# Optimization experiments

Hardware: AMD Instinct MI355X
Metric: run time of the kernel (lower is better)

## Reference

```python
import jax, jax.numpy as jnp
import numpy as np

B, D, H, L = 2, 1024, 16, 4
BLK = 16                 # block_size == max_text_tokens
MT, MF = 16, 2032        # max_text_tokens, max_font_tokens
S = MT + MF              # 2048
NB = S // BLK            # 128 blocks
V = 490                  # font_vocab_size
HD = D // H              # 64
WIN = 30                 # 3*max_glyph_tokens/block_size = 3*160/16
NGLOB, NRAND = 1, 2      # BigBird global / random blocks
SOS = 0.42


def _make_layout():
    # Deterministic BigBird block layout per head: [H, NB, NB] bool
    rng = np.random.default_rng(0)
    layout = np.zeros((H, NB, NB), dtype=bool)
    layout[:, :NGLOB, :] = True          # global rows
    layout[:, :, :NGLOB] = True          # global cols
    for i in range(NB):                  # sliding window
        layout[:, i, max(0, i - WIN // 2):min(NB, i + WIN // 2 + 1)] = True
    for h in range(H):                   # random blocks
        for i in range(NB):
            layout[h, i, rng.choice(NB, size=NRAND, replace=False)] = True
    return jnp.asarray(layout)


def setup_inputs() -> dict:
    key = jax.random.key(0)
    ks = jax.random.split(key, 16)
    p = lambda k, shape: (0.02 * jax.random.normal(k, shape)).astype(jnp.float32)
    return {
        "text_embeddings": jax.random.normal(ks[0], (B, MT, D), jnp.float32),
        "font_embeddings": jax.random.normal(ks[1], (B, MF, D), jnp.float32),
        "layout": _make_layout(),
        "Wq": p(ks[2], (L, D, D)), "bq": jnp.zeros((L, D), jnp.float32),
        "Wk": p(ks[3], (L, D, D)), "bk": jnp.zeros((L, D), jnp.float32),
        "Wv": p(ks[4], (L, D, D)), "bv": jnp.zeros((L, D), jnp.float32),
        "Wo": p(ks[5], (L, D, D)), "bo": jnp.zeros((L, D), jnp.float32),
        "ln1_g": jnp.ones((L, D), jnp.float32), "ln1_b": jnp.zeros((L, D), jnp.float32),
        "ln2_g": jnp.ones((L, D), jnp.float32), "ln2_b": jnp.zeros((L, D), jnp.float32),
        "W1": p(ks[6], (L, D, 4 * D)), "b1": jnp.zeros((L, 4 * D), jnp.float32),
        "W2": p(ks[7], (L, 4 * D, D)), "b2": jnp.zeros((L, D), jnp.float32),
        "lnf_g": jnp.ones((D,), jnp.float32), "lnf_b": jnp.zeros((D,), jnp.float32),
        "Wout": p(ks[8], (D, V)),
    }


def _ln(x, g, b, eps=1e-5):
    mu = x.mean(-1, keepdims=True)
    var = ((x - mu) ** 2).mean(-1, keepdims=True)
    return (x - mu) * jax.lax.rsqrt(var + eps) * g + b


def _forward(text_embeddings, font_embeddings, layout, Wq, bq, Wk, bk, Wv, bv, Wo, bo,
             ln1_g, ln1_b, ln2_g, ln2_b, W1, b1, W2, b2, lnf_g, lnf_b, Wout):
    sos = jnp.full((B, 1, D), SOS, text_embeddings.dtype)
    x = jnp.concatenate([sos, text_embeddings, font_embeddings[:, :-1, :]], axis=1)  # [B,S,D]
    # token-level mask = block-sparse BigBird layout AND causal -> [H,S,S]
    tok_mask = jnp.repeat(jnp.repeat(layout, BLK, axis=1), BLK, axis=2)
    tok_mask = tok_mask & jnp.tril(jnp.ones((S, S), bool))[None]
    neg = jnp.asarray(-1e9, x.dtype)
    scale = jnp.asarray(1.0 / np.sqrt(HD), x.dtype)

    def layer(x, p):
        wq, bq_, wk, bk_, wv, bv_, wo, bo_, g1, gb1, g2, gb2, w1, bb1, w2, bb2 = p
        q = (x @ wq + bq_).reshape(B, S, H, HD).transpose(0, 2, 1, 3)
        k = (x @ wk + bk_).reshape(B, S, H, HD).transpose(0, 2, 1, 3)
        v = (x @ wv + bv_).reshape(B, S, H, HD).transpose(0, 2, 1, 3)
        scores = jnp.einsum('bhqd,bhkd->bhqk', q, k) * scale
        scores = jnp.where(tok_mask[None], scores, neg)
        probs = jax.nn.softmax(scores, axis=-1)
        a = jnp.einsum('bhqk,bhkd->bhqd', probs, v).transpose(0, 2, 1, 3).reshape(B, S, D)
        a = a @ wo + bo_
        x = _ln(x + a, g1, gb1)                                   # post-norm residual
        m = jax.nn.gelu(x @ w1 + bb1, approximate=False) @ w2 + bb2  # dropout=eval no-op
        x = _ln(x + m, g2, gb2)
        return x, None

    params = (Wq, bq, Wk, bk, Wv, bv, Wo, bo, ln1_g, ln1_b, ln2_g, ln2_b, W1, b1, W2, b2)
    x, _ = jax.lax.scan(jax.checkpoint(layer), x, params)
    logits = _ln(x, lnf_g, lnf_b) @ Wout                          # [B,S,V]
    return logits[:, :MT, :], logits[:, MT:, :]


def reference(text_embeddings, font_embeddings, layout, Wq, bq, Wk, bk, Wv, bv, Wo, bo,
              ln1_g, ln1_b, ln2_g, ln2_b, W1, b1, W2, b2, lnf_g, lnf_b, Wout):
    return _forward(text_embeddings, font_embeddings, layout, Wq, bq, Wk, bk, Wv, bv, Wo, bo,
                    ln1_g, ln1_b, ln2_g, ln2_b, W1, b1, W2, b2, lnf_g, lnf_b, Wout)
```

## Files before the change

### kernel.cpp

```cpp
#include <hip/hip_runtime.h>
#include <hip/hip_bf16.h>
#include <math.h>


typedef __hip_bfloat16 bf16;
typedef __attribute__((ext_vector_type(8))) short bf16x8;
typedef __attribute__((ext_vector_type(8))) unsigned short us8;
typedef __attribute__((ext_vector_type(4))) unsigned short us4;
typedef __attribute__((ext_vector_type(4))) float f32x4;
typedef __attribute__((ext_vector_type(8))) _Float16 f16x8;

#define S_LEN 2048
#define D_MODEL 1024
#define NBLK 128
#define NHEAD 16
#define BATCH 2
#define M_ROWS 4096
#define VOCAB 490

__device__ __forceinline__ float ldw(const void* p, size_t i, bool bf) {
    return bf ? __bfloat162float(((const bf16*)p)[i]) : ((const float*)p)[i];
}
__device__ __forceinline__ bool is_bf(const unsigned* probe) {
    return probe[0] != 0x3F800000u;
}
__device__ __forceinline__ unsigned short f2b(float f) {
    union { float f; unsigned u; } x; x.f = f;
    return (unsigned short)((x.u + 0x7FFFu + ((x.u >> 16) & 1u)) >> 16);
}
__device__ __forceinline__ unsigned short f2h(float f) {
    union { _Float16 h; unsigned short u; } x; x.h = (_Float16)f;
    return x.u;
}
__device__ __forceinline__ unsigned packh(float a, float b) {
    return (unsigned)f2h(a) | ((unsigned)f2h(b) << 16);
}

__global__ __launch_bounds__(256) void norm_layout_kernel(
    const unsigned char* __restrict__ lraw, unsigned char* __restrict__ mask)
{
    int i = blockIdx.x * 256 + threadIdx.x;
    bool bytes_mode = (lraw[1] == 1);
    unsigned char v;
    if (bytes_mode) v = lraw[i] ? 1 : 0;
    else            v = ((const unsigned*)lraw)[i] ? 1 : 0;
    mask[i] = v;
}

__global__ __launch_bounds__(256) void build_x_kernel(
    const void* __restrict__ text, const void* __restrict__ font,
    float* __restrict__ x, unsigned short* __restrict__ xb,
    const unsigned* __restrict__ probe)
{
    bool bf = is_bf(probe);
    size_t idx = (size_t)blockIdx.x * 256 + threadIdx.x;
    int d = (int)(idx & 1023);
    int s = (int)((idx >> 10) & 2047);
    int b = (int)(idx >> 21);
    float v;
    if (s == 0)       v = bf ? 0.419921875f : 0.42f;
    else if (s <= 16) v = ldw(text, ((size_t)(b * 16 + (s - 1))) * 1024 + d, bf);
    else              v = ldw(font, ((size_t)(b * 2032 + (s - 17))) * 1024 + d, bf);
    x[idx] = v;
    xb[idx] = f2b(v);
}

__global__ __launch_bounds__(256) void transw_kernel(
    const void* __restrict__ W, size_t wOff, unsigned short* __restrict__ Wt,
    int K, int N, const unsigned* __restrict__ probe)
{
    bool bf = is_bf(probe);
    __shared__ unsigned short tile[32][34];
    int k0 = blockIdx.x * 32, n0 = blockIdx.y * 32;
    int t = threadIdx.x, c = t & 31, r0 = t >> 5;
    #pragma unroll
    for (int i = 0; i < 4; ++i) {
        int n = n0 + c;
        float v = (n < N) ? ldw(W, wOff + (size_t)(k0 + r0 + i * 8) * N + n, bf) : 0.f;
        tile[r0 + i * 8][c] = f2b(v);
    }
    __syncthreads();
    #pragma unroll
    for (int i = 0; i < 4; ++i)
        Wt[(size_t)(n0 + r0 + i * 8) * K + k0 + c] = tile[c][r0 + i * 8];
}

__global__ __launch_bounds__(256) void transw4_kernel(
    const void* __restrict__ Wa, const void* __restrict__ Wb,
    const void* __restrict__ Wc, const void* __restrict__ Wd,
    size_t wOff, unsigned short* __restrict__ wt,
    const unsigned* __restrict__ probe)
{
    bool bf = is_bf(probe);
    int z = blockIdx.z;
    const void* W = z == 0 ? Wa : (z == 1 ? Wb : (z == 2 ? Wc : Wd));
    unsigned short* Wt = wt + (size_t)z * (1u << 20);
    __shared__ unsigned short tile[32][34];
    int k0 = blockIdx.x * 32, n0 = blockIdx.y * 32;
    int t = threadIdx.x, c = t & 31, r0 = t >> 5;
    #pragma unroll
    for (int i = 0; i < 4; ++i) {
        float v = ldw(W, wOff + (size_t)(k0 + r0 + i * 8) * 1024 + n0 + c, bf);
        tile[r0 + i * 8][c] = f2b(v);
    }
    __syncthreads();
    #pragma unroll
    for (int i = 0; i < 4; ++i)
        Wt[(size_t)(n0 + r0 + i * 8) * 1024 + k0 + c] = tile[c][r0 + i * 8];
}

__global__ __launch_bounds__(512) void gemm_kernel(
    const unsigned short* __restrict__ Ab,
    const unsigned short* __restrict__ Wt, size_t wtStride,
    const void* __restrict__ b0, const void* __restrict__ b1p, const void* __restrict__ b2p,
    size_t bOff,
    float* __restrict__ C0, float* __restrict__ C1, float* __restrict__ C2,
    void* __restrict__ Cb0, void* __restrict__ Cb1, void* __restrict__ Cb2,
    int M, int N, int K, int act, int outmode, const unsigned* __restrict__ probe)
{
    bool bf = is_bf(probe);
    __shared__ __align__(16) unsigned short As[2][128 * 64];
    __shared__ __align__(16) unsigned short Bs[2][128 * 64];

    int t    = threadIdx.x;
    int lane = t & 63;
    int wid  = t >> 6;
    int wm   = wid >> 2;
    int wn   = wid & 3;

    int gx  = gridDim.x;
    int nwg = gx * gridDim.y;
    int bid = blockIdx.y * gx + blockIdx.x;
    int swz = (bid & 7) * (nwg >> 3) + (bid >> 3);
    int m0  = (swz / gx) * 128;
    int n0t = (swz % gx) * 128;
    int sel = n0t / N;
    int n0  = n0t - sel * N;

    const void* bias = sel == 0 ? b0 : (sel == 1 ? b1p : b2p);
    float* C         = sel == 0 ? C0 : (sel == 1 ? C1 : C2);
    void* Cb         = sel == 0 ? Cb0 : (sel == 1 ? Cb1 : Cb2);
    const unsigned short* Wtb = Wt + (size_t)sel * wtStride;
    const bool vtr = (outmode == 3 && sel == 2);

    f32x4 acc[4][2];
    #pragma unroll
    for (int i = 0; i < 4; i++)
        #pragma unroll
        for (int j = 0; j < 2; j++)
            acc[i][j] = (f32x4){0.f, 0.f, 0.f, 0.f};

    const int fm = lane & 15;

    auto stageA = [&](int bb, int kt) {
        int k0 = kt << 6;
        #pragma unroll
        for (int c = 0; c < 2; ++c) {
            int p    = (wid * 2 + c) * 64 + lane;
            int row  = p >> 3;
            int cp   = p & 7;
            int csrc = cp ^ (row & 7);
            const unsigned short* src = Ab + (size_t)(m0 + row) * K + k0 + csrc * 8;
            unsigned short* dst = &As[bb][(wid * 2 + c) * 512];
            __builtin_amdgcn_global_load_lds(
                (const __attribute__((address_space(1))) unsigned int*)src,
                (__attribute__((address_space(3))) unsigned int*)dst, 16, 0, 0);
        }
    };
    auto stageB = [&](int bb, int kt) {
        int k0 = kt << 6;
        #pragma unroll
        for (int c = 0; c < 2; ++c) {
            int p    = (wid * 2 + c) * 64 + lane;
            int row  = p >> 3;
            int cp   = p & 7;
            int csrc = cp ^ (row & 7);
            const unsigned short* src = Wtb + (size_t)(n0 + row) * K + k0 + csrc * 8;
            unsigned short* dst = &Bs[bb][(wid * 2 + c) * 512];
            __builtin_amdgcn_global_load_lds(
                (const __attribute__((address_space(1))) unsigned int*)src,
                (__attribute__((address_space(3))) unsigned int*)dst, 16, 0, 0);
        }
    };
    auto compute = [&](int bb) {
        #pragma unroll
        for (int kk = 0; kk < 2; ++kk) {
            int cq = kk * 4 + (lane >> 4);
            bf16x8 af[4], bfr[2];
            #pragma unroll
            for (int i = 0; i < 4; ++i) {
                int r = wm * 64 + i * 16 + fm;
                af[i] = *(const bf16x8*)(&As[bb][r * 64 + (cq ^ (r & 7)) * 8]);
            }
            #pragma unroll
            for (int j = 0; j < 2; ++j) {
                int n = wn * 32 + j * 16 + fm;
                bfr[j] = *(const bf16x8*)(&Bs[bb][n * 64 + (cq ^ (n & 7)) * 8]);
            }
            #pragma unroll
            for (int i = 0; i < 4; ++i)
                #pragma unroll
                for (int j = 0; j < 2; ++j)
                    acc[i][j] = __builtin_amdgcn_mfma_f32_16x16x32_bf16(
                        af[i], bfr[j], acc[i][j], 0, 0, 0);
        }
    };

    int nt = K >> 6;
    stageA(0, 0);
    stageB(0, 0);
    __syncthreads();

    for (int kt = 0; kt < nt; ++kt) {
        int cur = kt & 1;
        bool more = (kt + 1) < nt;
        if (more) { stageA(cur ^ 1, kt + 1); stageB(cur ^ 1, kt + 1); }
        compute(cur);
        __syncthreads();
    }

    int rq = (lane >> 4) * 4;
    #pragma unroll
    for (int j = 0; j < 2; ++j) {
        int n = n0 + wn * 32 + j * 16 + fm;
        if (n >= N) continue;
        float bv = bias ? ldw(bias, bOff + n, bf) : 0.f;
        #pragma unroll
        for (int i = 0; i < 4; ++i) {
            int mb = m0 + wm * 64 + i * 16 + rq;
            if (vtr) {
                us4 o;
                #pragma unroll
                for (int r = 0; r < 4; ++r) o[r] = f2h(acc[i][j][r] + bv);
                int bb2 = mb >> 11, s0 = mb & 2047, hh = n >> 6, dd = n & 63;
                *(us4*)(&((unsigned short*)Cb)[((((size_t)(bb2 * 16 + hh)) * 64 + dd) << 11) + s0]) = o;
                continue;
            }
            #pragma unroll
            for (int r = 0; r < 4; ++r) {
                int m = mb + r;
                float v = acc[i][j][r] + bv;
                if (act == 1) v = 0.5f * v * (1.f + erff(v * 0.70710678118654752f));
                if (outmode == 0) {
                    C[(size_t)m * N + n] = v;
                } else if (outmode == 2) {
                    ((unsigned short*)Cb)[(size_t)m * N + n] = f2b(v);
                } else if (outmode == 3) {
                    ((unsigned short*)Cb)[(size_t)m * N + n] = f2h(v);
                } else {
                    int b = m >> 11;
                    int s = m & 2047;
                    size_t dst;
                    if (s < 16) dst = ((size_t)(b * 16 + s)) * N + n;
                    else        dst = (size_t)(BATCH * 16) * N + ((size_t)(b * 2032 + (s - 16))) * N + n;
                    if (bf) ((unsigned short*)Cb)[dst] = f2b(v);
                    else    ((float*)Cb)[dst] = v;
                }
            }
        }
    }
}

__global__ __launch_bounds__(256) void attn_kernel(
    const unsigned short* __restrict__ q16, const unsigned short* __restrict__ k16,
    const unsigned short* __restrict__ v16t, const unsigned char* __restrict__ mask,
    unsigned short* __restrict__ ab)
{
    int qgrp = blockIdx.x;
    int h = blockIdx.y, b = blockIdx.z;

    __shared__ __align__(16) unsigned short ksd[64 * 64];
    __shared__ __align__(16) unsigned short vst[64 * 64];
    __shared__ unsigned char cflag[33];
    __shared__ unsigned char aclist[33];
    __shared__ int nac;

    int t = threadIdx.x, lane = t & 63, w = t >> 6;
    int qb = qgrp * 4 + w;
    const int fm = lane & 15, rq = lane >> 4;

    const unsigned char* mrow0 = mask + ((size_t)h * NBLK) * NBLK;

    if (t <= qgrp) {
        int jc = t;
        bool f = false;
        #pragma unroll
        for (int mb = 0; mb < 4; ++mb) {
            int j = jc * 4 + mb;
            #pragma unroll
            for (int ww = 0; ww < 4; ++ww) {
                int qq = qgrp * 4 + ww;
                f = f || ((j <= qq) && mrow0[qq * NBLK + j]);
            }
        }
        cflag[jc] = f ? 1 : 0;
    }
    __syncthreads();
    if (t == 0) {
        int n = 0;
        for (int jc = 0; jc <= qgrp; ++jc)
            if (cflag[jc]) aclist[n++] = (unsigned char)jc;
        nac = n;
    }

    int qrow = qb * 16 + fm;
    size_t qbase = ((size_t)(b * S_LEN + qrow)) * D_MODEL + h * 64;
    f16x8 qf0 = *(const f16x8*)(q16 + qbase + rq * 8);
    f16x8 qf1 = *(const f16x8*)(q16 + qbase + 32 + rq * 8);

    f32x4 O[4];
    #pragma unroll
    for (int c = 0; c < 4; ++c) O[c] = (f32x4){0.f, 0.f, 0.f, 0.f};
    float m_run = -1e30f, l_run = 0.f;
    const f16x8 hzero = (f16x8){0,0,0,0,0,0,0,0};

    __syncthreads();
    int nacl = nac;

    const int srow = t >> 2;
    const int sg   = (t & 3) * 2;
    const size_t vtbase = ((size_t)(b * NHEAD + h) * 64) * S_LEN;
    us8 kr0, kr1, vr0, vr1;

    auto loadKV = [&](int jc) {
        size_t kb = ((size_t)(b * S_LEN + jc * 64 + srow)) * D_MODEL + h * 64 + sg * 8;
        kr0 = *(const us8*)(k16 + kb);
        kr1 = *(const us8*)(k16 + kb + 8);
        size_t vb_ = vtbase + (size_t)srow * S_LEN + jc * 64 + sg * 8;
        vr0 = *(const us8*)(v16t + vb_);
        vr1 = *(const us8*)(v16t + vb_ + 8);
    };
    auto writeKV = [&]() {
        int p0 = (sg) ^ (srow & 7), p1 = (sg + 1) ^ (srow & 7);
        *(us8*)(&ksd[srow * 64 + p0 * 8]) = kr0;
        *(us8*)(&ksd[srow * 64 + p1 * 8]) = kr1;
        *(us8*)(&vst[srow * 64 + p0 * 8]) = vr0;
        *(us8*)(&vst[srow * 64 + p1 * 8]) = vr1;
    };

    if (nacl > 0) loadKV(aclist[0]);

    for (int ci = 0; ci < nacl; ++ci) {
        int jc = aclist[ci];
        __syncthreads();
        writeKV();
        if (ci + 1 < nacl) loadKV(aclist[ci + 1]);
        __syncthreads();

        #pragma unroll
        for (int mb = 0; mb < 4; ++mb) {
            int j = jc * 4 + mb;
            bool actv = (j <= qb) && mrow0[qb * NBLK + j];
            if (!actv) continue;

            int krow = mb * 16 + fm;
            f16x8 kf0 = *(const f16x8*)(&ksd[krow * 64 + ((0 * 4 + rq) ^ (krow & 7)) * 8]);
            f16x8 kf1 = *(const f16x8*)(&ksd[krow * 64 + ((1 * 4 + rq) ^ (krow & 7)) * 8]);
            f32x4 st = (f32x4){0.f, 0.f, 0.f, 0.f};
            st = __builtin_amdgcn_mfma_f32_16x16x32_f16(kf0, qf0, st, 0, 0, 0);
            st = __builtin_amdgcn_mfma_f32_16x16x32_f16(kf1, qf1, st, 0, 0, 0);

            float s[4];
            #pragma unroll
            for (int r = 0; r < 4; ++r) {
                s[r] = st[r] * 0.125f;
                if (j == qb && (rq * 4 + r) > fm) s[r] = -1e30f;
            }
            float mx = fmaxf(fmaxf(s[0], s[1]), fmaxf(s[2], s[3]));
            mx = fmaxf(mx, __shfl_xor(mx, 16));
            mx = fmaxf(mx, __shfl_xor(mx, 32));
            mx = fmaxf(m_run, mx);
            float al = expf(m_run - mx);
            float p[4]; float ls = 0.f;
            #pragma unroll
            for (int r = 0; r < 4; ++r) {
                p[r] = (s[r] < -1e29f) ? 0.f : expf(s[r] - mx);
                ls += p[r];
            }
            ls += __shfl_xor(ls, 16);
            ls += __shfl_xor(ls, 32);
            l_run = l_run * al + ls;
            m_run = mx;

            unsigned ph01 = packh(p[0], p[1]), ph23 = packh(p[2], p[3]);
            int s0 = fm + (((rq & 1) * 2) << 4);
            int s1 = s0 + 16;
            unsigned w0 = __shfl(ph01, s0), w1 = __shfl(ph23, s0);
            unsigned w2 = __shfl(ph01, s1), w3 = __shfl(ph23, s1);
            union { unsigned u[4]; f16x8 v; } pcv;
            pcv.u[0] = w0; pcv.u[1] = w1; pcv.u[2] = w2; pcv.u[3] = w3;
            f16x8 pa = (rq < 2) ? pcv.v : hzero;

            float al0 = __shfl(al, rq * 4 + 0), al1 = __shfl(al, rq * 4 + 1);
            float al2 = __shfl(al, rq * 4 + 2), al3 = __shfl(al, rq * 4 + 3);
            #pragma unroll
            for (int c = 0; c < 4; ++c) {
                O[c][0] *= al0; O[c][1] *= al1; O[c][2] *= al2; O[c][3] *= al3;
                f16x8 vb = hzero;
                if (rq < 2) {
                    int vrow = c * 16 + fm;
                    vb = *(const f16x8*)(&vst[vrow * 64 + ((mb * 2 + rq) ^ (vrow & 7)) * 8]);
                }
                O[c] = __builtin_amdgcn_mfma_f32_16x16x32_f16(pa, vb, O[c], 0, 0, 0);
            }
        }
    }

    float li0 = 1.f / __shfl(l_run, rq * 4 + 0);
    float li1 = 1.f / __shfl(l_run, rq * 4 + 1);
    float li2 = 1.f / __shfl(l_run, rq * 4 + 2);
    float li3 = 1.f / __shfl(l_run, rq * 4 + 3);
    size_t obase = ((size_t)(b * S_LEN + qb * 16)) * D_MODEL + h * 64;
    #pragma unroll
    for (int c = 0; c < 4; ++c) {
        ab[obase + (size_t)(rq * 4 + 0) * D_MODEL + c * 16 + fm] = f2b(O[c][0] * li0);
        ab[obase + (size_t)(rq * 4 + 1) * D_MODEL + c * 16 + fm] = f2b(O[c][1] * li1);
        ab[obase + (size_t)(rq * 4 + 2) * D_MODEL + c * 16 + fm] = f2b(O[c][2] * li2);
        ab[obase + (size_t)(rq * 4 + 3) * D_MODEL + c * 16 + fm] = f2b(O[c][3] * li3);
    }
}

__global__ __launch_bounds__(256) void add_ln_kernel(
    const float* __restrict__ xin, const float* __restrict__ res,
    float* __restrict__ xout, unsigned short* __restrict__ bfout,
    const void* __restrict__ g, size_t gOff,
    const void* __restrict__ bt, size_t bOff, const unsigned* __restrict__ probe)
{
    bool bf = is_bf(probe);
    int row = blockIdx.x;
    int t = threadIdx.x;
    __shared__ float red[4];

    float4 xv = ((const float4*)(xin + (size_t)row * D_MODEL))[t];
    if (res) {
        float4 rv = ((const float4*)(res + (size_t)row * D_MODEL))[t];
        xv.x += rv.x; xv.y += rv.y; xv.z += rv.z; xv.w += rv.w;
    }
    float s = xv.x + xv.y + xv.z + xv.w;
    for (int off = 32; off > 0; off >>= 1) s += __shfl_down(s, off);
    if ((t & 63) == 0) red[t >> 6] = s;
    __syncthreads();
    float mu = (red[0] + red[1] + red[2] + red[3]) * (1.f / 1024.f);
    __syncthreads();

    float d0 = xv.x - mu, d1 = xv.y - mu, d2 = xv.z - mu, d3 = xv.w - mu;
    float s2 = d0 * d0 + d1 * d1 + d2 * d2 + d3 * d3;
    for (int off = 32; off > 0; off >>= 1) s2 += __shfl_down(s2, off);
    if ((t & 63) == 0) red[t >> 6] = s2;
    __syncthreads();
    float var = (red[0] + red[1] + red[2] + red[3]) * (1.f / 1024.f);
    float rstd = rsqrtf(var + 1e-5f);

    int dbase = t * 4;
    float4 ov;
    ov.x = d0 * rstd * ldw(g, gOff + dbase + 0, bf) + ldw(bt, bOff + dbase + 0, bf);
    ov.y = d1 * rstd * ldw(g, gOff + dbase + 1, bf) + ldw(bt, bOff + dbase + 1, bf);
    ov.z = d2 * rstd * ldw(g, gOff + dbase + 2, bf) + ldw(bt, bOff + dbase + 2, bf);
    ov.w = d3 * rstd * ldw(g, gOff + dbase + 3, bf) + ldw(bt, bOff + dbase + 3, bf);
    ((float4*)(xout + (size_t)row * D_MODEL))[t] = ov;
    if (bfout) {
        us4 bv = { f2b(ov.x), f2b(ov.y), f2b(ov.z), f2b(ov.w) };
        *(us4*)(bfout + (size_t)row * D_MODEL + dbase) = bv;
    }
}

extern "C" void kernel_launch(void* const* d_in, const int* in_sizes, int n_in,
                              void* d_out, int out_size, void* d_ws, size_t ws_size,
                              hipStream_t stream) {
    const void* text  = d_in[0];
    const void* font  = d_in[1];
    const unsigned char* lraw = (const unsigned char*)d_in[2];
    const void* Wq    = d_in[3];
    const void* bq    = d_in[4];
    const void* Wk    = d_in[5];
    const void* bk    = d_in[6];
    const void* Wv    = d_in[7];
    const void* bv    = d_in[8];
    const void* Wo    = d_in[9];
    const void* bo_   = d_in[10];
    const void* ln1g  = d_in[11];
    const void* ln1b  = d_in[12];
    const void* ln2g  = d_in[13];
    const void* ln2b  = d_in[14];
    const void* W1    = d_in[15];
    const void* b1    = d_in[16];
    const void* W2    = d_in[17];
    const void* b2    = d_in[18];
    const void* lnfg  = d_in[19];
    const void* lnfb  = d_in[20];
    const void* Wout  = d_in[21];
    const unsigned* probe = (const unsigned*)d_in[11];

    const size_t Q = (size_t)M_ROWS * D_MODEL;
    float* ws = (float*)d_ws;
    float* x  = ws;
    float* G0 = ws + Q;
    unsigned short* q16 = (unsigned short*)(ws + 2 * Q);
    unsigned short* k16 = q16 + Q;
    unsigned short* v16 = k16 + Q;
    unsigned short* hb  = (unsigned short*)(ws + 2 * Q);
    unsigned short* xb  = (unsigned short*)(ws + 4 * Q);
    unsigned short* ab  = (unsigned short*)(ws + 4 * Q + Q / 2);
    unsigned char* mask = (unsigned char*)(ws + 5 * Q);
    unsigned short* wt  = (unsigned short*)((char*)d_ws + 5 * Q * 4 + 262144);

    norm_layout_kernel<<<(NHEAD * NBLK * NBLK) / 256, 256, 0, stream>>>(lraw, mask);
    build_x_kernel<<<(BATCH * S_LEN * D_MODEL) / 256, 256, 0, stream>>>(text, font, x, xb, probe);

    dim3 gQKV(3 * D_MODEL / 128, M_ROWS / 128);
    dim3 gD(D_MODEL / 128, M_ROWS / 128);
    dim3 gF(4 * D_MODEL / 128, M_ROWS / 128);
    dim3 gV((VOCAB + 127) / 128, M_ROWS / 128);

    const size_t MSZ = (size_t)1 << 20;

    for (int l = 0; l < 4; l++) {
        size_t wo  = (size_t)l * D_MODEL * D_MODEL;
        size_t bo1 = (size_t)l * D_MODEL;
        size_t w1o = (size_t)l * D_MODEL * 4 * D_MODEL;
        size_t b1o = (size_t)l * 4 * D_MODEL;

        transw4_kernel<<<dim3(32, 32, 4), 256, 0, stream>>>(Wq, Wk, Wv, Wo, wo, wt, probe);

        gemm_kernel<<<gQKV, 512, 0, stream>>>(xb, wt, MSZ, bq, bk, bv, bo1,
                                              nullptr, nullptr, nullptr, q16, k16, v16,
                                              M_ROWS, D_MODEL, D_MODEL, 0, 3, probe);
        attn_kernel<<<dim3(S_LEN / 64, NHEAD, BATCH), 256, 0, stream>>>(
            q16, k16, v16, mask, ab);
        gemm_kernel<<<gD, 512, 0, stream>>>(ab, wt + 3 * MSZ, 0, bo_, bo_, bo_, bo1,
                                            G0, G0, G0, nullptr, nullptr, nullptr,
                                            M_ROWS, D_MODEL, D_MODEL, 0, 0, probe);
        add_ln_kernel<<<M_ROWS, 256, 0, stream>>>(x, G0, x, xb, ln1g, bo1, ln1b, bo1, probe);

        transw_kernel<<<dim3(32, 128), 256, 0, stream>>>(W1, w1o, wt, D_MODEL, 4 * D_MODEL, probe);
        transw_kernel<<<dim3(128, 32), 256, 0, stream>>>(W2, w1o, wt + 4 * MSZ, 4 * D_MODEL, D_MODEL, probe);

        gemm_kernel<<<gF, 512, 0, stream>>>(xb, wt, 0, b1, b1, b1, b1o,
                                            nullptr, nullptr, nullptr, hb, hb, hb,
                                            M_ROWS, 4 * D_MODEL, D_MODEL, 1, 2, probe);
        gemm_kernel<<<gD, 512, 0, stream>>>(hb, wt + 4 * MSZ, 0, b2, b2, b2, bo1,
                                            G0, G0, G0, nullptr, nullptr, nullptr,
                                            M_ROWS, D_MODEL, 4 * D_MODEL, 0, 0, probe);
        add_ln_kernel<<<M_ROWS, 256, 0, stream>>>(x, G0, x, xb, ln2g, bo1, ln2b, bo1, probe);
    }

    add_ln_kernel<<<M_ROWS, 256, 0, stream>>>(x, nullptr, G0, ab, lnfg, 0, lnfb, 0, probe);
    transw_kernel<<<dim3(32, 16), 256, 0, stream>>>(Wout, 0, wt, D_MODEL, VOCAB, probe);
    gemm_kernel<<<gV, 512, 0, stream>>>(ab, wt, 0, nullptr, nullptr, nullptr, 0,
                                        nullptr, nullptr, nullptr, d_out, d_out, d_out,
                                        M_ROWS, VOCAB, D_MODEL, 0, 1, probe);
}
```

Before: 1.409 ms.

## Split-K the N=1024 output GEMMs and fold partial sums into add+LayerNorm

```diff
diff --git a/kernel.cpp b/kernel.cpp
--- a/kernel.cpp
+++ b/kernel.cpp
@@ -116,6 +116,7 @@
     size_t bOff,
     float* __restrict__ C0, float* __restrict__ C1, float* __restrict__ C2,
     void* __restrict__ Cb0, void* __restrict__ Cb1, void* __restrict__ Cb2,
+    float* __restrict__ Cp,
     int M, int N, int K, int act, int outmode, const unsigned* __restrict__ probe)
 {
     bool bf = is_bf(probe);
@@ -136,6 +137,9 @@
     int n0t = (swz % gx) * 128;
     int sel = n0t / N;
     int n0  = n0t - sel * N;
+    int zz  = blockIdx.z;
+    int Kit = K / gridDim.z;
+    int kbase = zz * Kit;
 
     const void* bias = sel == 0 ? b0 : (sel == 1 ? b1p : b2p);
     float* C         = sel == 0 ? C0 : (sel == 1 ? C1 : C2);
@@ -153,7 +157,7 @@
     const int fm = lane & 15;
 
     auto stageA = [&](int bb, int kt) {
-        int k0 = kt << 6;
+        int k0 = kbase + (kt << 6);
         #pragma unroll
         for (int c = 0; c < 2; ++c) {
             int p    = (wid * 2 + c) * 64 + lane;
@@ -168,7 +172,7 @@
         }
     };
     auto stageB = [&](int bb, int kt) {
-        int k0 = kt << 6;
+        int k0 = kbase + (kt << 6);
         #pragma unroll
         for (int c = 0; c < 2; ++c) {
             int p    = (wid * 2 + c) * 64 + lane;
@@ -206,7 +210,7 @@
         }
     };
 
-    int nt = K >> 6;
+    int nt = Kit >> 6;
     stageA(0, 0);
     stageB(0, 0);
     __syncthreads();
@@ -224,10 +228,16 @@
     for (int j = 0; j < 2; ++j) {
         int n = n0 + wn * 32 + j * 16 + fm;
         if (n >= N) continue;
-        float bv = bias ? ldw(bias, bOff + n, bf) : 0.f;
+        float bv = (bias && zz == 0) ? ldw(bias, bOff + n, bf) : 0.f;
         #pragma unroll
         for (int i = 0; i < 4; ++i) {
             int mb = m0 + wm * 64 + i * 16 + rq;
+            if (zz > 0) {
+                #pragma unroll
+                for (int r = 0; r < 4; ++r)
+                    Cp[(size_t)(mb + r) * N + n] = acc[i][j][r];
+                continue;
+            }
             if (vtr) {
                 us4 o;
                 #pragma unroll
@@ -422,6 +432,7 @@
 
 __global__ __launch_bounds__(256) void add_ln_kernel(
     const float* __restrict__ xin, const float* __restrict__ res,
+    const float* __restrict__ res2,
     float* __restrict__ xout, unsigned short* __restrict__ bfout,
     const void* __restrict__ g, size_t gOff,
     const void* __restrict__ bt, size_t bOff, const unsigned* __restrict__ probe)
@@ -434,6 +445,10 @@
     float4 xv = ((const float4*)(xin + (size_t)row * D_MODEL))[t];
     if (res) {
         float4 rv = ((const float4*)(res + (size_t)row * D_MODEL))[t];
+        xv.x += rv.x; xv.y += rv.y; xv.z += rv.z; xv.w += rv.w;
+    }
+    if (res2) {
+        float4 rv = ((const float4*)(res2 + (size_t)row * D_MODEL))[t];
         xv.x += rv.x; xv.y += rv.y; xv.z += rv.z; xv.w += rv.w;
     }
     float s = xv.x + xv.y + xv.z + xv.w;
@@ -504,15 +519,20 @@
     unsigned char* mask = (unsigned char*)(ws + 5 * Q);
     unsigned short* wt  = (unsigned short*)((char*)d_ws + 5 * Q * 4 + 262144);
 
+    const size_t baseEnd = 5 * Q * 4 + 262144 + 8 * ((size_t)1 << 20) * 2;
+    bool canSplit = ws_size >= baseEnd + Q * 4;
+    float* part = (float*)((char*)d_ws + baseEnd);
+
     norm_layout_kernel<<<(NHEAD * NBLK * NBLK) / 256, 256, 0, stream>>>(lraw, mask);
     build_x_kernel<<<(BATCH * S_LEN * D_MODEL) / 256, 256, 0, stream>>>(text, font, x, xb, probe);
 
     dim3 gQKV(3 * D_MODEL / 128, M_ROWS / 128);
-    dim3 gD(D_MODEL / 128, M_ROWS / 128);
+    dim3 gD(D_MODEL / 128, M_ROWS / 128, canSplit ? 2 : 1);
     dim3 gF(4 * D_MODEL / 128, M_ROWS / 128);
     dim3 gV((VOCAB + 127) / 128, M_ROWS / 128);
 
     const size_t MSZ = (size_t)1 << 20;
+    const float* r2 = canSplit ? part : nullptr;
 
     for (int l = 0; l < 4; l++) {
         size_t wo  = (size_t)l * D_MODEL * D_MODEL;
@@ -524,29 +544,34 @@
 
         gemm_kernel<<<gQKV, 512, 0, stream>>>(xb, wt, MSZ, bq, bk, bv, bo1,
                                               nullptr, nullptr, nullptr, q16, k16, v16,
+                                              nullptr,
                                               M_ROWS, D_MODEL, D_MODEL, 0, 3, probe);
         attn_kernel<<<dim3(S_LEN / 64, NHEAD, BATCH), 256, 0, stream>>>(
             q16, k16, v16, mask, ab);
         gemm_kernel<<<gD, 512, 0, stream>>>(ab, wt + 3 * MSZ, 0, bo_, bo_, bo_, bo1,
                                             G0, G0, G0, nullptr, nullptr, nullptr,
+                                            part,
                                             M_ROWS, D_MODEL, D_MODEL, 0, 0, probe);
-        add_ln_kernel<<<M_ROWS, 256, 0, stream>>>(x, G0, x, xb, ln1g, bo1, ln1b, bo1, probe);
+        add_ln_kernel<<<M_ROWS, 256, 0, stream>>>(x, G0, r2, x, xb, ln1g, bo1, ln1b, bo1, probe);
 
         transw_kernel<<<dim3(32, 128), 256, 0, stream>>>(W1, w1o, wt, D_MODEL, 4 * D_MODEL, probe);
         transw_kernel<<<dim3(128, 32), 256, 0, stream>>>(W2, w1o, wt + 4 * MSZ, 4 * D_MODEL, D_MODEL, probe);
 
         gemm_kernel<<<gF, 512, 0, stream>>>(xb, wt, 0, b1, b1, b1, b1o,
                                             nullptr, nullptr, nullptr, hb, hb, hb,
+                                            nullptr,
                                             M_ROWS, 4 * D_MODEL, D_MODEL, 1, 2, probe);
         gemm_kernel<<<gD, 512, 0, stream>>>(hb, wt + 4 * MSZ, 0, b2, b2, b2, bo1,
                                             G0, G0, G0, nullptr, nullptr, nullptr,
+                                            part,
                                             M_ROWS, D_MODEL, 4 * D_MODEL, 0, 0, probe);
-        add_ln_kernel<<<M_ROWS, 256, 0, stream>>>(x, G0, x, xb, ln2g, bo1, ln2b, bo1, probe);
-    }
-
-    add_ln_kernel<<<M_ROWS, 256, 0, stream>>>(x, nullptr, G0, ab, lnfg, 0, lnfb, 0, probe);
+        add_ln_kernel<<<M_ROWS, 256, 0, stream>>>(x, G0, r2, x, xb, ln2g, bo1, ln2b, bo1, probe);
+    }
+
+    add_ln_kernel<<<M_ROWS, 256, 0, stream>>>(x, nullptr, nullptr, G0, ab, lnfg, 0, lnfb, 0, probe);
     transw_kernel<<<dim3(32, 16), 256, 0, stream>>>(Wout, 0, wt, D_MODEL, VOCAB, probe);
     gemm_kernel<<<gV, 512, 0, stream>>>(ab, wt, 0, nullptr, nullptr, nullptr, 0,
                                         nullptr, nullptr, nullptr, d_out, d_out, d_out,
+                                        nullptr,
                                         M_ROWS, VOCAB, D_MODEL, 0, 1, probe);
 }
```

New measurement: 1.332 ms. 1.06x faster.
